# Optimization experiments

Hardware: AMD Instinct MI355X
Metric: run time of the kernel (lower is better)

Reference implementation:

```python
import jax, jax.numpy as jnp
import numpy as np

B = 2048

def _conv(x, w, b, stride):
    y = jax.lax.conv_general_dilated(x, w, (stride, stride), 'VALID',
                                     dimension_numbers=('NCHW', 'OIHW', 'NCHW'))
    return y + b[None, :, None, None]

def _local_conv(x, w, b):
    # w: (Ho, Wo, Co, Ci, kh, kw), b: (Ho, Wo, Co); stride 1, valid
    Ho, Wo, Co, Ci, kh, kw = w.shape
    # patches: (B, Ci, kh*kw, Ho, Wo) -- sliding windows, small fixed loop over kernel taps
    patches = jnp.stack([x[:, :, i:i + Ho, j:j + Wo]
                         for i in range(kh) for j in range(kw)], axis=2)
    wf = w.reshape(Ho, Wo, Co, Ci, kh * kw)
    y = jnp.einsum('bcphw,hwocp->bohw', patches, wf)
    return y + jnp.transpose(b, (2, 0, 1))[None]

def setup_inputs() -> dict:
    key = jax.random.key(0)
    ks = jax.random.split(key, 18)
    s = 0.05
    inp = {
        'x': jax.random.normal(ks[0], (B, 5, 60, 60), dtype=jnp.float32),
        'info': jax.random.normal(ks[1], (B, 8), dtype=jnp.float32),
        'w1': jax.random.normal(ks[2], (32, 5, 3, 3), dtype=jnp.float32) * s,
        'b1': jnp.zeros((32,), dtype=jnp.float32),
        'w2a': jax.random.normal(ks[3], (64, 32, 3, 3), dtype=jnp.float32) * s,
        'b2a': jnp.zeros((64,), dtype=jnp.float32),
        'w2b': jax.random.normal(ks[4], (64, 64, 3, 3), dtype=jnp.float32) * s,
        'b2b': jnp.zeros((64,), dtype=jnp.float32),
        'lw3': jax.random.normal(ks[5], (9, 9, 64, 64, 5, 5), dtype=jnp.float32) * s,
        'lb3': jnp.zeros((9, 9, 64), dtype=jnp.float32),
        'lw4': jax.random.normal(ks[6], (5, 5, 64, 64, 5, 5), dtype=jnp.float32) * s,
        'lb4': jnp.zeros((5, 5, 64), dtype=jnp.float32),
        'lw5': jax.random.normal(ks[7], (3, 3, 64, 64, 3, 3), dtype=jnp.float32) * s,
        'lb5': jnp.zeros((3, 3, 64), dtype=jnp.float32),
        'hw': jax.random.normal(ks[8], (2, 584), dtype=jnp.float32) * s,
        'hb': jnp.zeros((2,), dtype=jnp.float32),
    }
    return inp

def reference(x, info, w1, b1, w2a, b2a, w2b, b2b, lw3, lb3, lw4, lb4, lw5, lb5, hw, hb):
    h = jnp.tanh(_conv(x, w1, b1, 2))            # (B,32,29,29)
    h = jnp.tanh(_conv(h, w2a, b2a, 1))          # (B,64,27,27)
    h = jnp.tanh(_conv(h, w2b, b2b, 2))          # (B,64,13,13)
    h = jnp.tanh(_local_conv(h, lw3, lb3))       # (B,64,9,9)
    h = jnp.tanh(_local_conv(h, lw4, lb4))       # (B,64,5,5)
    h = jnp.tanh(_local_conv(h, lw5, lb5))       # (B,64,3,3)
    h = h.reshape(h.shape[0], -1)                # (B,576)
    h = jnp.concatenate([h, info], axis=1)       # (B,584)
    logits = h @ hw.T + hb                       # (B,2)
    return jax.nn.softmax(logits, axis=1)
```

## Files before the change

### kernel.cpp

```cpp
#include <hip/hip_runtime.h>
#include <stdint.h>

#define THREADS 256

typedef short bf16x8 __attribute__((ext_vector_type(8)));
typedef float f32x4 __attribute__((ext_vector_type(4)));
typedef unsigned uint2_ __attribute__((ext_vector_type(2)));

#define GPTR(x) ((const __attribute__((address_space(1))) void*)(x))
#define LPTR(x) ((__attribute__((address_space(3))) void*)(x))

__device__ __forceinline__ unsigned short f2bf(float v) {
  unsigned u = __builtin_bit_cast(unsigned, v);
  u = (u + 0x7fff + ((u >> 16) & 1)) >> 16;
  return (unsigned short)u;
}
__device__ __forceinline__ float bf2f(unsigned short h) {
  return __builtin_bit_cast(float, (unsigned)h << 16);
}
__device__ __forceinline__ float fast_tanh(float x) {
  return 1.f - 2.f / (__expf(2.f * x) + 1.f);
}

__device__ __forceinline__ int xcd_swizzle(int wg, int nwg) {
  const int q = nwg >> 3, rr = nwg & 7;
  const int xcd = wg & 7, l = wg >> 3;
  return (xcd < rr ? xcd * (q + 1) : rr * (q + 1) + (xcd - rr) * q) + l;
}

__global__ void pack_w1t(const float* __restrict__ w1, float* __restrict__ w1t) {
  int idx = blockIdx.x * THREADS + threadIdx.x;
  if (idx >= 45 * 32) return;
  int t = idx >> 5, co = idx & 31;
  w1t[t * 32 + co] = w1[co * 45 + t];
}

__global__ void __launch_bounds__(256) conv1_direct(
    const float* __restrict__ x, const float* __restrict__ w1t,
    const float* __restrict__ bias, unsigned short* __restrict__ out, int Bc,
    int bstart) {
  constexpr int CI = 5, CO = 32, IH = 60, IW = 60, OH = 29, OW = 29;
  constexpr int RPB = 2, NRB = 15;

  __shared__ float xs[CI * 5 * 60];

  const int tid = threadIdx.x;
  const int b = blockIdx.x / NRB;
  const int qb = blockIdx.x % NRB;
  const int oh0 = qb * RPB;
  const int rows = min(RPB, OH - oh0);
  const int ih0 = oh0 * 2;
  const int ihn = rows * 2 + 1;

  const float* xp = x + (size_t)(bstart + b) * (CI * IH * IW);

  const int nf4 = CI * ihn * 15;
  for (int i = tid; i < nf4; i += 256) {
    int col = i % 15;
    int row = i / 15;
    int ci = row / ihn, r = row % ihn;
    ((float4*)xs)[row * 15 + col] = ((const float4*)xp)[(ci * IH + ih0 + r) * 15 + col];
  }
  __syncthreads();

  const int lane = tid & 63;
  const int wu = __builtin_amdgcn_readfirstlane(tid >> 6);
  if (lane >= rows * OW) return;
  const int r = lane / OW, c = lane % OW;
  const int base = (r * 2) * 60 + c * 2;
  const int cstr = ihn * 60;

  float acc[8];
#pragma unroll
  for (int j = 0; j < 8; j++) acc[j] = bias[wu * 8 + j];

#pragma unroll
  for (int ci = 0; ci < CI; ci++)
#pragma unroll
    for (int kh = 0; kh < 3; kh++)
#pragma unroll
      for (int kw = 0; kw < 3; kw++) {
        const float v = xs[ci * cstr + base + kh * 60 + kw];
        const float* wt = w1t + ((ci * 3 + kh) * 3 + kw) * 32 + wu * 8;
#pragma unroll
        for (int j = 0; j < 8; j++) acc[j] = fmaf(v, wt[j], acc[j]);
      }

  const int p = (oh0 + r) * OW + c;
  bf16x8 o;
#pragma unroll
  for (int j = 0; j < 8; j++) o[j] = (short)f2bf(fast_tanh(acc[j]));
  *(bf16x8*)(out + ((size_t)p * Bc + b) * CO + wu * 8) = o;
}

template <int CI, int KS>
__global__ void __launch_bounds__(THREADS) pack_w(const float* __restrict__ w,
                                                  unsigned short* __restrict__ wp,
                                                  int npos) {
  constexpr int K = CI * KS * KS;
  constexpr int S = K / 32;
  int idx = blockIdx.x * THREADS + threadIdx.x;
  int total = npos * S * 2048;
  if (idx >= total) return;
  int e = idx & 7;
  int lane = (idx >> 3) & 63;
  int mt = (idx >> 9) & 3;
  int rest = idx >> 11;
  int s = rest % S, pos = rest / S;
  int co = mt * 16 + (lane & 15);
  int k = s * 32 + (lane >> 4) * 8 + e;
  int tap = k / CI, ci = k % CI;
  int kh = tap / KS, kw = tap % KS;
  float v = w[((((size_t)pos * 64 + co) * CI + ci) * KS + kh) * KS + kw];
  wp[idx] = f2bf(v);
}

template <int CI, int IH, int IW, int OH, int OW, int KS, int ST, bool LOCAL, int BT>
__global__ void __launch_bounds__(256) conv_mfma(
    const unsigned short* __restrict__ X, const unsigned short* __restrict__ Wp,
    const float* __restrict__ bias, unsigned short* __restrict__ Y, int Bc) {
  constexpr int S = CI * KS * KS / 32;
  constexpr int NPOS = OH * OW;
  constexpr int NJ = BT / 64;
  constexpr int NB = BT / 64;

  __shared__ unsigned short As[2][2048];
  __shared__ unsigned short Bs[2][BT * 32];

  const int tid = threadIdx.x;
  const int lane = tid & 63;
  const int wu = tid >> 6;
  const int n = lane & 15, g = lane >> 4;

  const int nbt = Bc / BT;
  int wg = xcd_swizzle(blockIdx.x, gridDim.x);
  int pos, btile;
  if (LOCAL) {
    btile = wg % nbt;
    pos = wg / nbt;
  } else {
    pos = wg % NPOS;
    btile = wg / NPOS;
  }
  const int oh = pos / OW, ow = pos % OW;
  const int b0 = btile * BT;

  const unsigned short* Wpp = Wp + (LOCAL ? (size_t)pos * (S * 2048) : 0);

  const int srow = tid >> 2;
  const int scol = (tid & 3) * 8;

  auto stage = [&](int s, int buf) {
    __builtin_amdgcn_global_load_lds(GPTR(Wpp + s * 2048 + tid * 8),
                                     LPTR(&As[buf][tid * 8]), 16, 0, 0);
    const int tap = (s * 32) / CI;
    const int ci0 = (s * 32) % CI;
    const int kh = tap / KS, kw = tap % KS;
    const int pin = (oh * ST + kh) * IW + (ow * ST + kw);
    const size_t base = (size_t)pin * Bc + b0;
#pragma unroll
    for (int i = 0; i < NB; i++)
      __builtin_amdgcn_global_load_lds(
          GPTR(X + (base + i * 64 + srow) * CI + ci0 + scol),
          LPTR(&Bs[buf][i * 2048 + tid * 8]), 16, 0, 0);
  };

  f32x4 acc[4][NJ] = {};

  stage(0, 0);
  int buf = 0;
  for (int s = 0; s < S; s++) {
    __syncthreads();
    if (s + 1 < S) stage(s + 1, buf ^ 1);

    bf16x8 bfr[NJ];
#pragma unroll
    for (int j = 0; j < NJ; j++) {
      const int local_b = wu * (NJ * 16) + j * 16 + n;
      bfr[j] = *(const bf16x8*)(&Bs[buf][local_b * 32 + g * 8]);
    }
    bf16x8 af[4];
#pragma unroll
    for (int mt = 0; mt < 4; mt++)
      af[mt] = *(const bf16x8*)(&As[buf][(mt * 64 + lane) * 8]);

#pragma unroll
    for (int mt = 0; mt < 4; mt++)
#pragma unroll
      for (int j = 0; j < NJ; j++)
        acc[mt][j] =
            __builtin_amdgcn_mfma_f32_16x16x32_bf16(af[mt], bfr[j], acc[mt][j], 0, 0, 0);
    buf ^= 1;
  }

#pragma unroll
  for (int mt = 0; mt < 4; mt++) {
#pragma unroll
    for (int j = 0; j < NJ; j++) {
      unsigned short o[4];
#pragma unroll
      for (int r = 0; r < 4; r++) {
        const int co = mt * 16 + g * 4 + r;
        o[r] = f2bf(fast_tanh(acc[mt][j][r] +
                              (LOCAL ? bias[pos * 64 + co] : bias[co])));
      }
      const int b = b0 + wu * (NJ * 16) + j * 16 + n;
      uint2_ pk;
      pk[0] = (unsigned)o[0] | ((unsigned)o[1] << 16);
      pk[1] = (unsigned)o[2] | ((unsigned)o[3] << 16);
      *(uint2_*)(Y + ((size_t)pos * Bc + b) * 64 + mt * 16 + g * 4) = pk;
    }
  }
}

__global__ void head_k(const unsigned short* __restrict__ h5,
                       const float* __restrict__ info, const float* __restrict__ hw,
                       const float* __restrict__ hb, float* __restrict__ out, int Bc,
                       int bstart) {
  int b = blockIdx.x * THREADS + threadIdx.x;
  if (b >= Bc) return;
  float l0 = hb[0], l1 = hb[1];
  for (int pos = 0; pos < 9; pos++) {
#pragma unroll
    for (int cb = 0; cb < 8; cb++) {
      bf16x8 v8 = *(const bf16x8*)(h5 + ((size_t)pos * Bc + b) * 64 + cb * 8);
#pragma unroll
      for (int j = 0; j < 8; j++) {
        float v = bf2f((unsigned short)v8[j]);
        int f = (cb * 8 + j) * 9 + pos;
        l0 = fmaf(v, hw[f], l0);
        l1 = fmaf(v, hw[584 + f], l1);
      }
    }
  }
#pragma unroll
  for (int k = 0; k < 8; k++) {
    float v = info[(size_t)(bstart + b) * 8 + k];
    l0 = fmaf(v, hw[576 + k], l0);
    l1 = fmaf(v, hw[584 + 576 + k], l1);
  }
  float m = fmaxf(l0, l1);
  float e0 = __expf(l0 - m), e1 = __expf(l1 - m);
  float s = e0 + e1;
  out[(size_t)(bstart + b) * 2 + 0] = e0 / s;
  out[(size_t)(bstart + b) * 2 + 1] = e1 / s;
}


extern "C" void kernel_launch(void* const* d_in, const int* in_sizes, int n_in,
                              void* d_out, int out_size, void* d_ws, size_t ws_size,
                              hipStream_t stream) {
  const float* x = (const float*)d_in[0];
  const float* info = (const float*)d_in[1];
  const float* w1 = (const float*)d_in[2];
  const float* b1 = (const float*)d_in[3];
  const float* w2a = (const float*)d_in[4];
  const float* b2a = (const float*)d_in[5];
  const float* w2b = (const float*)d_in[6];
  const float* b2b = (const float*)d_in[7];
  const float* lw3 = (const float*)d_in[8];
  const float* lb3 = (const float*)d_in[9];
  const float* lw4 = (const float*)d_in[10];
  const float* lb4 = (const float*)d_in[11];
  const float* lw5 = (const float*)d_in[12];
  const float* lb5 = (const float*)d_in[13];
  const float* hw = (const float*)d_in[14];
  const float* hb = (const float*)d_in[15];
  float* out = (float*)d_out;

  const int B = in_sizes[0] / 18000;

  const size_t SZ2A = 9ull * 2048, SZ2B = 18ull * 2048, SZ3 = 81ull * 50 * 2048,
               SZ4 = 25ull * 50 * 2048, SZ5 = 9ull * 18 * 2048;
  unsigned short* wp2a = (unsigned short*)d_ws;
  unsigned short* wp2b = wp2a + SZ2A;
  unsigned short* wp3 = wp2b + SZ2B;
  unsigned short* wp4 = wp3 + SZ3;
  unsigned short* wp5 = wp4 + SZ4;
  size_t wp_bytes = (SZ2A + SZ2B + SZ3 + SZ4 + SZ5) * 2;
  wp_bytes = (wp_bytes + 255) & ~(size_t)255;
  float* w1t = (float*)((char*)d_ws + wp_bytes);
  size_t w1t_bytes = ((45 * 32 * 4) + 255) & ~(size_t)255;

  const size_t PSA = 53824, PSB = 93312;
  const size_t per_sample = PSA + PSB;
  int Bc = B;
  while (Bc > 256 && wp_bytes + w1t_bytes + (size_t)Bc * per_sample + 4096 > ws_size)
    Bc >>= 1;

  char* base = (char*)d_ws + wp_bytes + w1t_bytes;
  unsigned short* bufA = (unsigned short*)base;
  unsigned short* bufB = (unsigned short*)(base + (size_t)Bc * PSA);

  hipLaunchKernelGGL(pack_w1t, dim3(6), dim3(THREADS), 0, stream, w1, w1t);
  hipLaunchKernelGGL((pack_w<32, 3>), dim3((SZ2A + 255) / 256), dim3(THREADS), 0, stream,
                     w2a, wp2a, 1);
  hipLaunchKernelGGL((pack_w<64, 3>), dim3((SZ2B + 255) / 256), dim3(THREADS), 0, stream,
                     w2b, wp2b, 1);
  hipLaunchKernelGGL((pack_w<64, 5>), dim3((SZ3 + 255) / 256), dim3(THREADS), 0, stream,
                     lw3, wp3, 81);
  hipLaunchKernelGGL((pack_w<64, 5>), dim3((SZ4 + 255) / 256), dim3(THREADS), 0, stream,
                     lw4, wp4, 25);
  hipLaunchKernelGGL((pack_w<64, 3>), dim3((SZ5 + 255) / 256), dim3(THREADS), 0, stream,
                     lw5, wp5, 9);

  const int nchunks = B / Bc;
  for (int c = 0; c < nchunks; c++) {
    const int bstart = c * Bc;

    hipLaunchKernelGGL(conv1_direct, dim3(Bc * 15), dim3(256), 0, stream, x, w1t, b1,
                       bufA, Bc, bstart);
    hipLaunchKernelGGL((conv_mfma<32, 29, 29, 27, 27, 3, 1, false, 256>),
                       dim3(729 * (Bc / 256)), dim3(256), 0, stream, bufA, wp2a, b2a,
                       bufB, Bc);
    hipLaunchKernelGGL((conv_mfma<64, 27, 27, 13, 13, 3, 2, false, 256>),
                       dim3(169 * (Bc / 256)), dim3(256), 0, stream, bufB, wp2b, b2b,
                       bufA, Bc);
    hipLaunchKernelGGL((conv_mfma<64, 13, 13, 9, 9, 5, 1, true, 256>),
                       dim3(81 * (Bc / 256)), dim3(256), 0, stream, bufA, wp3, lb3, bufB,
                       Bc);
    hipLaunchKernelGGL((conv_mfma<64, 9, 9, 5, 5, 5, 1, true, 128>),
                       dim3(25 * (Bc / 128)), dim3(256), 0, stream, bufB, wp4, lb4, bufA,
                       Bc);
    hipLaunchKernelGGL((conv_mfma<64, 5, 5, 3, 3, 3, 1, true, 128>),
                       dim3(9 * (Bc / 128)), dim3(256), 0, stream, bufA, wp5, lb5, bufB,
                       Bc);
    hipLaunchKernelGGL(head_k, dim3((Bc + THREADS - 1) / THREADS), dim3(THREADS), 0,
                       stream, bufB, info, hw, hb, out, Bc, bstart);
  }
}
```

Before: 537.6 us.

## Add conv2a kernel keeping full weight panel in LDS across nine output positions

Adds a dedicated kernel for the conv2a layer. It loads all nine weight k-slices into LDS once per workgroup, then loops over a run of nine output positions, pipelining the B-tile loads across positions. This replaces one block per output position and cuts the number of blocks nine-fold, which removes repeated weight staging and per-block launch overhead. It also swaps the multiplies by Bc and CI in address math for shifts, which assumes Bc is a power of two. The cost is 68 KB of dynamic LDS per block, which limits occupancy, and longer serial work per block.

New measurement: 549.7 us. 1.02x slower.

```diff
diff --git a/kernel.cpp b/kernel.cpp
--- a/kernel.cpp
+++ b/kernel.cpp
@@ -115,14 +115,112 @@
   wp[idx] = f2bf(v);
 }
 
+__global__ void __launch_bounds__(256) conv2a_apanel(
+    const unsigned short* __restrict__ X, const unsigned short* __restrict__ Wp,
+    const float* __restrict__ bias, unsigned short* __restrict__ Y, int Bc,
+    int bcsh) {
+  constexpr int S = 9, OW = 27, IW = 29;
+  extern __shared__ unsigned short sm[];
+  unsigned short* As = sm;
+  unsigned short* Bs = sm + 9 * 2048;
+
+  const int tid = threadIdx.x;
+  const int lane = tid & 63;
+  const int wu = tid >> 6;
+  const int n = lane & 15, g = lane >> 4;
+
+  const int nbt = Bc >> 8;
+  int wg = xcd_swizzle(blockIdx.x, gridDim.x);
+  const int prun = wg % 81;
+  const int btile = wg / 81;
+  const int oh = prun / 3;
+  const int ow0 = (prun % 3) * 9;
+  const int b0 = btile * 256;
+  (void)nbt;
+
+#pragma unroll
+  for (int s = 0; s < S; s++)
+    __builtin_amdgcn_global_load_lds(GPTR(Wp + s * 2048 + tid * 8),
+                                     LPTR(As + s * 2048 + tid * 8), 16, 0, 0);
+
+  const int srow = tid >> 2;
+  const int scol = (tid & 3) * 8;
+
+  auto stageB = [&](int pidx2, int s2, int buf) {
+    const int kh = s2 / 3, kw = s2 % 3;
+    const int pin = (oh + kh) * IW + ow0 + pidx2 + kw;
+    const size_t base = ((size_t)pin << bcsh) + b0;
+#pragma unroll
+    for (int i = 0; i < 4; i++)
+      __builtin_amdgcn_global_load_lds(
+          GPTR(X + (((base + i * 64 + srow)) << 5) + scol),
+          LPTR(Bs + buf * 8192 + i * 2048 + tid * 8), 16, 0, 0);
+  };
+
+  stageB(0, 0, 0);
+
+  int buf = 0;
+  for (int pidx = 0; pidx < 9; pidx++) {
+    f32x4 acc[4][4] = {};
+#pragma unroll
+    for (int s = 0; s < S; s++) {
+      __syncthreads();
+      if (s < 8)
+        stageB(pidx, s + 1, buf ^ 1);
+      else if (pidx + 1 < 9)
+        stageB(pidx + 1, 0, buf ^ 1);
+
+      bf16x8 bfr[4];
+#pragma unroll
+      for (int j = 0; j < 4; j++) {
+        const int local_b = wu * 64 + j * 16 + n;
+        bfr[j] = *(const bf16x8*)(Bs + buf * 8192 + local_b * 32 + g * 8);
+      }
+      bf16x8 af[4];
+#pragma unroll
+      for (int mt = 0; mt < 4; mt++)
+        af[mt] = *(const bf16x8*)(As + s * 2048 + (mt * 64 + lane) * 8);
+
+#pragma unroll
+      for (int mt = 0; mt < 4; mt++)
+#pragma unroll
+        for (int j = 0; j < 4; j++)
+          acc[mt][j] = __builtin_amdgcn_mfma_f32_16x16x32_bf16(af[mt], bfr[j],
+                                                               acc[mt][j], 0, 0, 0);
+      buf ^= 1;
+    }
+
+    const int pos = oh * OW + ow0 + pidx;
+#pragma unroll
+    for (int mt = 0; mt < 4; mt++) {
+#pragma unroll
+      for (int j = 0; j < 4; j++) {
+        unsigned short o[4];
+#pragma unroll
+        for (int r = 0; r < 4; r++) {
+          const int co = mt * 16 + g * 4 + r;
+          o[r] = f2bf(fast_tanh(acc[mt][j][r] + bias[co]));
+        }
+        const int b = b0 + wu * 64 + j * 16 + n;
+        uint2_ pk;
+        pk[0] = (unsigned)o[0] | ((unsigned)o[1] << 16);
+        pk[1] = (unsigned)o[2] | ((unsigned)o[3] << 16);
+        *(uint2_*)(Y + (((size_t)pos << bcsh) + b) * 64 + mt * 16 + g * 4) = pk;
+      }
+    }
+  }
+}
+
 template <int CI, int IH, int IW, int OH, int OW, int KS, int ST, bool LOCAL, int BT>
 __global__ void __launch_bounds__(256) conv_mfma(
     const unsigned short* __restrict__ X, const unsigned short* __restrict__ Wp,
-    const float* __restrict__ bias, unsigned short* __restrict__ Y, int Bc) {
+    const float* __restrict__ bias, unsigned short* __restrict__ Y, int Bc,
+    int bcsh) {
   constexpr int S = CI * KS * KS / 32;
   constexpr int NPOS = OH * OW;
   constexpr int NJ = BT / 64;
   constexpr int NB = BT / 64;
+  constexpr int CISH = (CI == 64) ? 6 : 5;
 
   __shared__ unsigned short As[2][2048];
   __shared__ unsigned short Bs[2][BT * 32];
@@ -157,11 +255,11 @@
     const int ci0 = (s * 32) % CI;
     const int kh = tap / KS, kw = tap % KS;
     const int pin = (oh * ST + kh) * IW + (ow * ST + kw);
-    const size_t base = (size_t)pin * Bc + b0;
+    const size_t base = ((size_t)pin << bcsh) + b0;
 #pragma unroll
     for (int i = 0; i < NB; i++)
       __builtin_amdgcn_global_load_lds(
-          GPTR(X + (base + i * 64 + srow) * CI + ci0 + scol),
+          GPTR(X + ((base + i * 64 + srow) << CISH) + ci0 + scol),
           LPTR(&Bs[buf][i * 2048 + tid * 8]), 16, 0, 0);
   };
 
@@ -208,7 +306,7 @@
       uint2_ pk;
       pk[0] = (unsigned)o[0] | ((unsigned)o[1] << 16);
       pk[1] = (unsigned)o[2] | ((unsigned)o[3] << 16);
-      *(uint2_*)(Y + ((size_t)pos * Bc + b) * 64 + mt * 16 + g * 4) = pk;
+      *(uint2_*)(Y + (((size_t)pos << bcsh) + b) * 64 + mt * 16 + g * 4) = pk;
     }
   }
 }
@@ -246,6 +344,12 @@
   out[(size_t)(bstart + b) * 2 + 1] = e1 / s;
 }
 
+
+static inline int ilog2i(int v) {
+  int s = 0;
+  while ((1 << s) < v) s++;
+  return s;
+}
 
 extern "C" void kernel_launch(void* const* d_in, const int* in_sizes, int n_in,
                               void* d_out, int out_size, void* d_ws, size_t ws_size,
@@ -287,6 +391,7 @@
   int Bc = B;
   while (Bc > 256 && wp_bytes + w1t_bytes + (size_t)Bc * per_sample + 4096 > ws_size)
     Bc >>= 1;
+  const int bcsh = ilog2i(Bc);
 
   char* base = (char*)d_ws + wp_bytes + w1t_bytes;
   unsigned short* bufA = (unsigned short*)base;
@@ -310,21 +415,20 @@
 
     hipLaunchKernelGGL(conv1_direct, dim3(Bc * 15), dim3(256), 0, stream, x, w1t, b1,
                        bufA, Bc, bstart);
-    hipLaunchKernelGGL((conv_mfma<32, 29, 29, 27, 27, 3, 1, false, 256>),
-                       dim3(729 * (Bc / 256)), dim3(256), 0, stream, bufA, wp2a, b2a,
-                       bufB, Bc);
+    hipLaunchKernelGGL(conv2a_apanel, dim3(81 * (Bc / 256)), dim3(256), 69632, stream,
+                       bufA, wp2a, b2a, bufB, Bc, bcsh);
     hipLaunchKernelGGL((conv_mfma<64, 27, 27, 13, 13, 3, 2, false, 256>),
                        dim3(169 * (Bc / 256)), dim3(256), 0, stream, bufB, wp2b, b2b,
-                       bufA, Bc);
+                       bufA, Bc, bcsh);
     hipLaunchKernelGGL((conv_mfma<64, 13, 13, 9, 9, 5, 1, true, 256>),
                        dim3(81 * (Bc / 256)), dim3(256), 0, stream, bufA, wp3, lb3, bufB,
-                       Bc);
+                       Bc, bcsh);
     hipLaunchKernelGGL((conv_mfma<64, 9, 9, 5, 5, 5, 1, true, 128>),
                        dim3(25 * (Bc / 128)), dim3(256), 0, stream, bufB, wp4, lb4, bufA,
-                       Bc);
+                       Bc, bcsh);
     hipLaunchKernelGGL((conv_mfma<64, 5, 5, 3, 3, 3, 1, true, 128>),
                        dim3(9 * (Bc / 128)), dim3(256), 0, stream, bufA, wp5, lb5, bufB,
-                       Bc);
+                       Bc, bcsh);
     hipLaunchKernelGGL(head_k, dim3((Bc + THREADS - 1) / THREADS), dim3(THREADS), 0,
                        stream, bufB, info, hw, hb, out, Bc, bstart);
   }
```
